# Performance work log

Measured on AMD Instinct MI355X. Metric: run time of the kernel, lower is better.

## Reference

```python
import jax, jax.numpy as jnp
import numpy as np

N = 100000   # nodes
E = 1600000  # edges
S = 4        # state_dimension
H = 64       # hidden_channels


def _gcn_conv(x, row, col, W, b):
    """PyG GCNConv: h = x @ W; add self-loops; symmetric deg^-1/2 norm; scatter-add; + bias."""
    n = x.shape[0]
    h = x @ W  # [N, out]
    loop = jnp.arange(n, dtype=row.dtype)
    r = jnp.concatenate([row, loop])  # sources (with self-loops)
    c = jnp.concatenate([col, loop])  # targets (with self-loops)
    deg = jax.ops.segment_sum(jnp.ones(r.shape[0], h.dtype), c, num_segments=n)
    dinv = jnp.where(deg > 0, jax.lax.rsqrt(deg), 0.0)
    norm = dinv[r] * dinv[c]                      # [E+N]
    msg = h[r] * norm[:, None]                    # gather + scale, [E+N, out]
    out = jax.ops.segment_sum(msg, c, num_segments=n)  # scatter-add
    return out + b


def setup_inputs() -> dict:
    key = jax.random.key(0)
    k1, k2, k3, k4 = jax.random.split(key, 4)
    x = jax.random.normal(k1, (N, S), dtype=jnp.float32)
    edge_index = jax.random.randint(k2, (2, E), 0, N, dtype=jnp.int32)
    # Glorot-ish init for the two GCNConv linear layers (+ zero bias, PyG default)
    W1 = jax.random.normal(k3, (S, H), dtype=jnp.float32) * (1.0 / np.sqrt(S))
    b1 = jnp.zeros((H,), jnp.float32)
    W2 = jax.random.normal(k4, (H, S), dtype=jnp.float32) * (1.0 / np.sqrt(H))
    b2 = jnp.zeros((S,), jnp.float32)
    return {"x": x, "edge_index": edge_index, "W1": W1, "b1": b1, "W2": W2, "b2": b2}


def reference(x, edge_index, W1, b1, W2, b2):
    row, col = edge_index[0], edge_index[1]
    h = _gcn_conv(x, row, col, W1, b1)
    h = jax.nn.relu(h)
    out = _gcn_conv(h, row, col, W2, b2)
    return out
```

## Files before the change

kernel.cpp:

```cpp
#include <hip/hip_runtime.h>


#define CSHIFT 10
#define CNODES 1024
#define KC_MAX 128
#define CAPC   18432
#define EPB    4096
#define PTH    512
#define CURPAD 16
#define HCAP   9216
#define ANODES 128
#define ACAP   2432

__global__ void k_zero(int* __restrict__ p, int n) {
    int i = blockIdx.x * blockDim.x + threadIdx.x;
    if (i < n) p[i] = 0;
}

__global__ void __launch_bounds__(PTH) k_part(
        const int* __restrict__ row, const int* __restrict__ col,
        int e, int Kc, int* __restrict__ cursor, unsigned* __restrict__ ere) {
    __shared__ int wh[8][KC_MAX];
    __shared__ int h[KC_MAX];
    __shared__ int loff[KC_MAX];
    __shared__ int gbase[KC_MAX];
    __shared__ unsigned staged[EPB];
    int t = threadIdx.x, w = t >> 6;
    for (int k = t; k < 8 * KC_MAX; k += PTH) ((int*)wh)[k] = 0;
    __syncthreads();
    int lo = blockIdx.x * EPB;
    int cbuf[8], rbuf[8];
#pragma unroll
    for (int k = 0; k < 8; ++k) {
        int i = lo + t + k * PTH;
        if (i < e) { cbuf[k] = col[i]; rbuf[k] = row[i]; }
        else { cbuf[k] = -1; rbuf[k] = 0; }
    }
#pragma unroll
    for (int k = 0; k < 8; ++k)
        if (cbuf[k] >= 0) atomicAdd(&wh[w][cbuf[k] >> CSHIFT], 1);
    __syncthreads();
    if (t < KC_MAX) {
        int s = 0;
#pragma unroll
        for (int w2 = 0; w2 < 8; ++w2) s += wh[w2][t];
        h[t] = s;
        loff[t] = s;
    }
    __syncthreads();
    for (int off = 1; off < KC_MAX; off <<= 1) {
        int v = (t < KC_MAX && t >= off) ? loff[t - off] : 0;
        __syncthreads();
        if (t < KC_MAX) loff[t] += v;
        __syncthreads();
    }
    if (t < KC_MAX) {
        int st = loff[t] - h[t];
        loff[t] = st;
        if (t < Kc && h[t]) gbase[t] = atomicAdd(&cursor[t * CURPAD], h[t]);
        int run = st;
#pragma unroll
        for (int w2 = 0; w2 < 8; ++w2) { int c = wh[w2][t]; wh[w2][t] = run; run += c; }
    }
    __syncthreads();
#pragma unroll
    for (int k = 0; k < 8; ++k) {
        int c = cbuf[k];
        if (c < 0) continue;
        int pos = atomicAdd(&wh[w][c >> CSHIFT], 1);
        staged[pos] = ((unsigned)rbuf[k] << CSHIFT) | (unsigned)(c & (CNODES - 1));
    }
    __syncthreads();
    int lane = t & 63;
    for (int k = w; k < Kc; k += 8) {
        int len = h[k];
        if (!len) continue;
        int gb = gbase[k], lb = loff[k];
        size_t dst = (size_t)k * CAPC + gb;
        for (int j = lane; j < len; j += 64)
            if (gb + j < CAPC) ere[dst + j] = staged[lb + j];
    }
}

__global__ void __launch_bounds__(1024) k_sortH(
        const int* __restrict__ cursor, unsigned* __restrict__ ere,
        int* __restrict__ rstart, const float4* __restrict__ x,
        float* __restrict__ dinv, float4* __restrict__ y, int n) {
    __shared__ int hist[CNODES];
    __shared__ int scn[CNODES];
    __shared__ int cur[CNODES];
    __shared__ unsigned sorted[HCAP];
    int bh = blockIdx.x, b = bh >> 1, h = bh & 1;
    int t = threadIdx.x, nlo = b << CSHIFT;
    hist[t] = 0;
    __syncthreads();
    size_t c0 = (size_t)b * CAPC;
    int m = min(cursor[b * CURPAD], CAPC);
    int n4 = m >> 2;
    const uint4* e4 = (const uint4*)(ere + c0);
    uint4 rb[5];
    int gv[5];
#pragma unroll
    for (int k = 0; k < 5; ++k) {
        int g = t + k * 1024;
        gv[k] = (g < n4);
        if (gv[k]) rb[k] = e4[g];
    }
    unsigned tailrec = 0xFFFFFFFFu;
    {
        int ti = (n4 << 2) + t;
        if (ti < m) tailrec = ere[c0 + ti];
    }
#pragma unroll
    for (int k = 0; k < 5; ++k) {
        if (!gv[k]) continue;
        atomicAdd(&hist[rb[k].x & (CNODES - 1)], 1);
        atomicAdd(&hist[rb[k].y & (CNODES - 1)], 1);
        atomicAdd(&hist[rb[k].z & (CNODES - 1)], 1);
        atomicAdd(&hist[rb[k].w & (CNODES - 1)], 1);
    }
    if (tailrec != 0xFFFFFFFFu) atomicAdd(&hist[tailrec & (CNODES - 1)], 1);
    __syncthreads();
    int hv = hist[t];
    scn[t] = hv;
    __syncthreads();
    for (int off = 1; off < CNODES; off <<= 1) {
        int v = (t >= off) ? scn[t - off] : 0;
        __syncthreads();
        scn[t] += v;
        __syncthreads();
    }
    int st = scn[t] - hv;
    int low = scn[CNODES / 2 - 1];
    rstart[(b << CSHIFT) + t] = (int)c0 + st;
    int base = h ? low : 0;
    cur[t] = st - base;
    if ((t >> 9) == h) {
        int node = nlo + t;
        if (node < n) {
            float di = rsqrtf((float)hv + 1.0f);
            dinv[node] = di;
            float4 xv = x[node];
            y[node] = make_float4(xv.x * di, xv.y * di, xv.z * di, xv.w * di);
        }
    }
    __syncthreads();
#pragma unroll
    for (int k = 0; k < 5; ++k) {
        if (!gv[k]) continue;
        unsigned e0 = rb[k].x, e1 = rb[k].y, e2 = rb[k].z, e3 = rb[k].w;
        int l0 = e0 & (CNODES - 1);
        if ((l0 >> 9) == h) { int p = atomicAdd(&cur[l0], 1); if (p < HCAP) sorted[p] = e0 >> CSHIFT; }
        int l1 = e1 & (CNODES - 1);
        if ((l1 >> 9) == h) { int p = atomicAdd(&cur[l1], 1); if (p < HCAP) sorted[p] = e1 >> CSHIFT; }
        int l2 = e2 & (CNODES - 1);
        if ((l2 >> 9) == h) { int p = atomicAdd(&cur[l2], 1); if (p < HCAP) sorted[p] = e2 >> CSHIFT; }
        int l3 = e3 & (CNODES - 1);
        if ((l3 >> 9) == h) { int p = atomicAdd(&cur[l3], 1); if (p < HCAP) sorted[p] = e3 >> CSHIFT; }
    }
    if (tailrec != 0xFFFFFFFFu) {
        int l = tailrec & (CNODES - 1);
        if ((l >> 9) == h) { int p = atomicAdd(&cur[l], 1); if (p < HCAP) sorted[p] = tailrec >> CSHIFT; }
    }
    __syncthreads();
    int cnt = h ? (m - low) : low;
    int wb = min(cnt, HCAP);
    for (int i = t; i < wb; i += 1024) ere[c0 + base + i] = sorted[i];
}

__global__ void __launch_bounds__(512) k_mid(
        const unsigned* __restrict__ ere, const int* __restrict__ rstart,
        const int* __restrict__ cursor, const float* __restrict__ dinv,
        const float4* __restrict__ x, const float4* __restrict__ y,
        const float* __restrict__ W1, const float* __restrict__ b1,
        const float* __restrict__ W2, const float* __restrict__ b2,
        float4* __restrict__ z, float4* __restrict__ out, int n) {
    __shared__ unsigned recs[ACAP];
    __shared__ float4 sums[ANODES];
    int g = blockIdx.x, t = threadIdx.x;
    int nlo = g * ANODES;
    int b = nlo >> CSHIFT;
    int c0i = (int)((size_t)b * CAPC);
    int s0 = rstart[nlo];
    int e0 = ((g & 7) == 7) ? c0i + min(cursor[b * CURPAD], CAPC)
                            : rstart[nlo + ANODES];
    int len = min(e0 - s0, ACAP);
    for (int i = t; i < len; i += 512) recs[i] = ere[s0 + i];
    __syncthreads();
    int tt = t >> 2, q = t & 3;
    int s = rstart[nlo + tt] - s0;
    int epos = (tt == ANODES - 1) ? len : min(rstart[nlo + tt + 1] - s0, len);
    float vx = 0.f, vy = 0.f, vz = 0.f, vw = 0.f;
    int i = s + q;
    while (i + 12 < epos) {
        int r0 = recs[i], r1 = recs[i + 4], r2 = recs[i + 8], r3 = recs[i + 12];
        float4 a0 = y[r0], a1 = y[r1], a2 = y[r2], a3 = y[r3];
        vx += a0.x + a1.x + a2.x + a3.x;
        vy += a0.y + a1.y + a2.y + a3.y;
        vz += a0.z + a1.z + a2.z + a3.z;
        vw += a0.w + a1.w + a2.w + a3.w;
        i += 16;
    }
    for (; i < epos; i += 4) {
        float4 a = y[recs[i]];
        vx += a.x; vy += a.y; vz += a.z; vw += a.w;
    }
    vx += __shfl_xor(vx, 1); vx += __shfl_xor(vx, 2);
    vy += __shfl_xor(vy, 1); vy += __shfl_xor(vy, 2);
    vz += __shfl_xor(vz, 1); vz += __shfl_xor(vz, 2);
    vw += __shfl_xor(vw, 1); vw += __shfl_xor(vw, 2);
    if (q == 0) sums[tt] = make_float4(vx, vy, vz, vw);
    __syncthreads();
    int node = nlo + t;
    if (t < ANODES && node < n) {
        float di = dinv[node], sl = di * di;
        float4 sv = sums[t];
        float4 xv = x[node];
        float a0 = di * sv.x + xv.x * sl;
        float a1 = di * sv.y + xv.y * sl;
        float a2 = di * sv.z + xv.z * sl;
        float a3 = di * sv.w + xv.w * sl;
        float t0 = 0.f, t1 = 0.f, t2 = 0.f, t3 = 0.f;
#pragma unroll 8
        for (int j = 0; j < 64; ++j) {
            float hh = b1[j] + a0 * W1[j] + a1 * W1[64 + j] + a2 * W1[128 + j] + a3 * W1[192 + j];
            hh = fmaxf(hh, 0.f);
            t0 += hh * W2[j * 4 + 0];
            t1 += hh * W2[j * 4 + 1];
            t2 += hh * W2[j * 4 + 2];
            t3 += hh * W2[j * 4 + 3];
        }
        z[node] = make_float4(t0 * di, t1 * di, t2 * di, t3 * di);
        out[node] = make_float4(b2[0] + t0 * sl, b2[1] + t1 * sl,
                                b2[2] + t2 * sl, b2[3] + t3 * sl);
    }
}

__global__ void __launch_bounds__(512) k_acc2(
        const unsigned* __restrict__ ere, const int* __restrict__ rstart,
        const int* __restrict__ cursor, const float* __restrict__ dinv,
        const float4* __restrict__ z, float4* __restrict__ out, int n) {
    __shared__ unsigned recs[ACAP];
    __shared__ float4 sums[ANODES];
    int g = blockIdx.x, t = threadIdx.x;
    int nlo = g * ANODES;
    int b = nlo >> CSHIFT;
    int c0i = (int)((size_t)b * CAPC);
    int s0 = rstart[nlo];
    int e0 = ((g & 7) == 7) ? c0i + min(cursor[b * CURPAD], CAPC)
                            : rstart[nlo + ANODES];
    int len = min(e0 - s0, ACAP);
    for (int i = t; i < len; i += 512) recs[i] = ere[s0 + i];
    __syncthreads();
    int tt = t >> 2, q = t & 3;
    int s = rstart[nlo + tt] - s0;
    int epos = (tt == ANODES - 1) ? len : min(rstart[nlo + tt + 1] - s0, len);
    float vx = 0.f, vy = 0.f, vz = 0.f, vw = 0.f;
    int i = s + q;
    while (i + 12 < epos) {
        int r0 = recs[i], r1 = recs[i + 4], r2 = recs[i + 8], r3 = recs[i + 12];
        float4 a0 = z[r0], a1 = z[r1], a2 = z[r2], a3 = z[r3];
        vx += a0.x + a1.x + a2.x + a3.x;
        vy += a0.y + a1.y + a2.y + a3.y;
        vz += a0.z + a1.z + a2.z + a3.z;
        vw += a0.w + a1.w + a2.w + a3.w;
        i += 16;
    }
    for (; i < epos; i += 4) {
        float4 a = z[recs[i]];
        vx += a.x; vy += a.y; vz += a.z; vw += a.w;
    }
    vx += __shfl_xor(vx, 1); vx += __shfl_xor(vx, 2);
    vy += __shfl_xor(vy, 1); vy += __shfl_xor(vy, 2);
    vz += __shfl_xor(vz, 1); vz += __shfl_xor(vz, 2);
    vw += __shfl_xor(vw, 1); vw += __shfl_xor(vw, 2);
    if (q == 0) sums[tt] = make_float4(vx, vy, vz, vw);
    __syncthreads();
    int node = nlo + t;
    if (t < ANODES && node < n) {
        float di = dinv[node];
        float4 sv = sums[t];
        float4 o = out[node];
        out[node] = make_float4(o.x + di * sv.x, o.y + di * sv.y,
                                o.z + di * sv.z, o.w + di * sv.w);
    }
}

extern "C" void kernel_launch(void* const* d_in, const int* in_sizes, int n_in,
                              void* d_out, int out_size, void* d_ws, size_t ws_size,
                              hipStream_t stream) {
    const float* x  = (const float*)d_in[0];
    const int* edge = (const int*)d_in[1];
    const float* W1 = (const float*)d_in[2];
    const float* b1 = (const float*)d_in[3];
    const float* W2 = (const float*)d_in[4];
    const float* b2 = (const float*)d_in[5];
    float* out = (float*)d_out;

    const int n = in_sizes[0] / 4;
    const int e = in_sizes[1] / 2;
    const int* row = edge;
    const int* col = edge + e;
    const int Kc = (n + CNODES - 1) >> CSHIFT;

    char* ws = (char*)d_ws;
    float* y    = (float*)ws;  ws += (size_t)4 * n * 4;
    float* zmid = (float*)ws;  ws += (size_t)4 * n * 4;
    float* dinv = (float*)ws;  ws += (size_t)n * 4;
    unsigned* ere = (unsigned*)ws;  ws += (size_t)Kc * CAPC * 4;
    int* cursor = (int*)ws;    ws += (size_t)Kc * CURPAD * 4;
    int* rstart = (int*)ws;    ws += (size_t)Kc * CNODES * 4;

    const int B = 256;
    const int gp = (e + EPB - 1) / EPB;
    const int ga = (n + ANODES - 1) / ANODES;
    const int nz = Kc * CURPAD;

    k_zero<<<(nz + B - 1) / B, B, 0, stream>>>(cursor, nz);
    k_part<<<gp, PTH, 0, stream>>>(row, col, e, Kc, cursor, ere);
    k_sortH<<<2 * Kc, 1024, 0, stream>>>(cursor, ere, rstart, (const float4*)x,
                                         dinv, (float4*)y, n);
    k_mid<<<ga, 512, 0, stream>>>(ere, rstart, cursor, dinv, (const float4*)x,
                                  (const float4*)y, W1, b1, W2, b2,
                                  (float4*)zmid, (float4*)out, n);
    k_acc2<<<ga, 512, 0, stream>>>(ere, rstart, cursor, dinv,
                                   (const float4*)zmid, (float4*)out, n);
}
```

Baseline: 126.9 us.

## Drop shared staging in edge partition, scatter directly to bucket slots

The partition kernel no longer stages edges in shared memory or runs a block-wide prefix scan. Each bucket reserves its global range with one atomic, and each wave's shared counter is seeded with that global base so edges are written straight to their final slots. The block is halved to 256 threads and 2048 edges to shrink shared memory and raise occupancy. The price is scattered, uncoalesced 4-byte global writes in place of contiguous per-bucket copies, and twice as many blocks issuing global cursor atomics.

```diff
diff --git a/kernel.cpp b/kernel.cpp
--- a/kernel.cpp
+++ b/kernel.cpp
@@ -5,8 +5,8 @@
 #define CNODES 1024
 #define KC_MAX 128
 #define CAPC   18432
-#define EPB    4096
-#define PTH    512
+#define EPB    2048
+#define PTH    256
 #define CURPAD 16
 #define HCAP   9216
 #define ANODES 128
@@ -20,13 +20,9 @@
 __global__ void __launch_bounds__(PTH) k_part(
         const int* __restrict__ row, const int* __restrict__ col,
         int e, int Kc, int* __restrict__ cursor, unsigned* __restrict__ ere) {
-    __shared__ int wh[8][KC_MAX];
-    __shared__ int h[KC_MAX];
-    __shared__ int loff[KC_MAX];
-    __shared__ int gbase[KC_MAX];
-    __shared__ unsigned staged[EPB];
+    __shared__ int wh[4][KC_MAX];
     int t = threadIdx.x, w = t >> 6;
-    for (int k = t; k < 8 * KC_MAX; k += PTH) ((int*)wh)[k] = 0;
+    for (int k = t; k < 4 * KC_MAX; k += PTH) ((int*)wh)[k] = 0;
     __syncthreads();
     int lo = blockIdx.x * EPB;
     int cbuf[8], rbuf[8];
@@ -41,44 +37,23 @@
         if (cbuf[k] >= 0) atomicAdd(&wh[w][cbuf[k] >> CSHIFT], 1);
     __syncthreads();
     if (t < KC_MAX) {
-        int s = 0;
-#pragma unroll
-        for (int w2 = 0; w2 < 8; ++w2) s += wh[w2][t];
-        h[t] = s;
-        loff[t] = s;
-    }
-    __syncthreads();
-    for (int off = 1; off < KC_MAX; off <<= 1) {
-        int v = (t < KC_MAX && t >= off) ? loff[t - off] : 0;
-        __syncthreads();
-        if (t < KC_MAX) loff[t] += v;
-        __syncthreads();
-    }
-    if (t < KC_MAX) {
-        int st = loff[t] - h[t];
-        loff[t] = st;
-        if (t < Kc && h[t]) gbase[t] = atomicAdd(&cursor[t * CURPAD], h[t]);
-        int run = st;
-#pragma unroll
-        for (int w2 = 0; w2 < 8; ++w2) { int c = wh[w2][t]; wh[w2][t] = run; run += c; }
+        int s = wh[0][t] + wh[1][t] + wh[2][t] + wh[3][t];
+        int gb = 0;
+        if (t < Kc && s) gb = atomicAdd(&cursor[t * CURPAD], s);
+        int run = gb;
+#pragma unroll
+        for (int w2 = 0; w2 < 4; ++w2) { int c = wh[w2][t]; wh[w2][t] = run; run += c; }
     }
     __syncthreads();
 #pragma unroll
     for (int k = 0; k < 8; ++k) {
         int c = cbuf[k];
         if (c < 0) continue;
-        int pos = atomicAdd(&wh[w][c >> CSHIFT], 1);
-        staged[pos] = ((unsigned)rbuf[k] << CSHIFT) | (unsigned)(c & (CNODES - 1));
-    }
-    __syncthreads();
-    int lane = t & 63;
-    for (int k = w; k < Kc; k += 8) {
-        int len = h[k];
-        if (!len) continue;
-        int gb = gbase[k], lb = loff[k];
-        size_t dst = (size_t)k * CAPC + gb;
-        for (int j = lane; j < len; j += 64)
-            if (gb + j < CAPC) ere[dst + j] = staged[lb + j];
+        int b = c >> CSHIFT;
+        int pos = atomicAdd(&wh[w][b], 1);
+        if (pos < CAPC)
+            ere[(size_t)b * CAPC + pos] =
+                ((unsigned)rbuf[k] << CSHIFT) | (unsigned)(c & (CNODES - 1));
     }
 }
 
```

After: 136.9 us. 1.08x slower.
